# Kernel optimization log

Hardware: AMD Instinct MI355X
Metric: run time of the kernel (lower is better)

## Reference

```python
import jax, jax.numpy as jnp
import numpy as np

N_R = 256          # number of relations
N_HOP_MAX = 3      # max hops
N_E = 200_000      # number of entities
N_T = 1_000_000    # number of KB triples
B = 32             # batch size
D_Q = 768          # BERT question embedding dim
D_IN = D_Q + (N_HOP_MAX - 1) * N_R  # input width of dense_inf / dense_att


def setup_inputs() -> dict:
    key = jax.random.key(0)
    ks = jax.random.split(key, 7)
    x = (jax.random.uniform(ks[0], (B, N_E)) < 0.001).astype(jnp.float32)
    h_q = jax.random.normal(ks[1], (B, D_Q), jnp.float32)
    W_inf = jax.random.normal(ks[2], (N_R, D_IN), jnp.float32) * 0.02
    W_att = jax.random.normal(ks[3], (1, D_IN), jnp.float32) * 0.02
    subj_idx = jax.random.randint(ks[4], (N_T,), 0, N_E, jnp.int32)
    rel_idx = jax.random.randint(ks[5], (N_T,), 0, N_R, jnp.int32)
    obj_idx = jax.random.randint(ks[6], (N_T,), 0, N_E, jnp.int32)
    return {"x": x, "h_q": h_q, "W_inf": W_inf, "W_att": W_att,
            "subj_idx": subj_idx, "rel_idx": rel_idx, "obj_idx": obj_idx,
            "n_hop": N_HOP_MAX}


def _one_step(x, r, subj_idx, rel_idx, obj_idx):
    # Equivalent to ((x @ M_subj.T) * (r @ M_rel.T)) @ M_obj with 0/1
    # indicator matrices: gather - elementwise multiply - scatter-add.
    x_t = jnp.take(x, subj_idx, axis=1)   # (B, N_T)
    r_t = jnp.take(r, rel_idx, axis=1)    # (B, N_T)
    prod = x_t * r_t                       # (B, N_T)
    # scatter-add over triples into object entities: (N_T, B) -> (N_E, B)
    return jax.ops.segment_sum(prod.T, obj_idx, num_segments=x.shape[1]).T


def reference(x, h_q, W_inf, W_att, subj_idx, rel_idx, obj_idx, n_hop):
    rs, cs, xs = [], [], []
    for i in range(n_hop):
        if i:
            # most-recent relation first, then older ones (rs[::-1])
            concat = jnp.concatenate([h_q] + rs[::-1], axis=1)
        else:
            concat = h_q
        pad = jnp.zeros((h_q.shape[0], (N_HOP_MAX - 1 - i) * N_R), h_q.dtype)
        concat = jnp.concatenate([concat, pad], axis=1)  # (B, D_IN)
        r = concat @ W_inf.T   # (B, N_R)
        c = concat @ W_att.T   # (B, 1)
        x = _one_step(x, r, subj_idx, rel_idx, obj_idx)  # (B, N_E)
        rs.append(r)
        cs.append(c)
        xs.append(x)
    a = jax.nn.softmax(jnp.concatenate(cs, axis=1), axis=-1)  # (B, n_hop)
    y = jnp.einsum('bh,bhe->be', a, jnp.stack(xs, axis=1))     # (B, N_E)
    return y
```

## Files before the change

### kernel.cpp

```cpp
#include <hip/hip_runtime.h>

#define N_R   256
#define N_E   200000
#define N_T   1000000
#define B     32
#define D_Q   768
#define D_IN  1280

__global__ void k_prep(const float* __restrict__ x, unsigned* __restrict__ mask0,
                       unsigned* __restrict__ mask1, unsigned* __restrict__ mask2,
                       float4* __restrict__ outv) {
    int tid = blockIdx.x * 256 + threadIdx.x;
    float4 z = {0.f, 0.f, 0.f, 0.f};
    outv[tid] = z;
    outv[800000 + tid] = z;
    if (tid < N_E) {
        unsigned m = 0;
#pragma unroll 8
        for (int b = 0; b < 32; ++b)
            m |= (x[(size_t)b * N_E + tid] != 0.f ? 1u : 0u) << b;
        mask0[tid] = m;
        mask1[tid] = 0u;
        mask2[tid] = 0u;
    }
}

__global__ void k_r0(const float* __restrict__ h_q, const float* __restrict__ W_inf,
                     float* __restrict__ rT0) {
    __shared__ float hs[32 * 257];
    __shared__ float red[256];
    int t = threadIdx.x, rel = blockIdx.x;
    int b = t & 31, kp = t >> 5;
    float acc = 0.f;
    for (int c = 0; c < 3; ++c) {
        __syncthreads();
#pragma unroll
        for (int i = 0; i < 32; ++i)
            hs[i * 257 + t] = h_q[i * D_Q + c * 256 + t];
        __syncthreads();
        const float* w = &W_inf[rel * D_IN + c * 256 + kp * 32];
#pragma unroll
        for (int i = 0; i < 32; ++i)
            acc += w[i] * hs[b * 257 + kp * 32 + i];
    }
    red[t] = acc;
    __syncthreads();
    if (t < 32) {
        float s = 0.f;
        for (int q = 0; q < 8; ++q) s += red[q * 32 + t];
        rT0[rel * 32 + t] = s;
    }
}

__global__ void k_r12(const float* __restrict__ W_inf, const float* __restrict__ rT0,
                      const float* __restrict__ rPrev, float* __restrict__ rOut,
                      int hop2, const float* __restrict__ a_scale) {
    __shared__ float red[256];
    int t = threadIdx.x, rel = blockIdx.x;
    int b = t & 31, jp = t >> 5;
    const float* w2 = &W_inf[rel * D_IN + D_Q];
    float acc = 0.f;
#pragma unroll 8
    for (int jj = 0; jj < 32; ++jj) {
        int j = jp * 32 + jj;
        acc += w2[j] * rPrev[j * 32 + b];
    }
    if (hop2) {
        const float* w3 = w2 + N_R;
#pragma unroll 8
        for (int jj = 0; jj < 32; ++jj) {
            int j = jp * 32 + jj;
            acc += w3[j] * rT0[j * 32 + b];
        }
    }
    red[t] = acc;
    __syncthreads();
    if (t < 32) {
        float s = rT0[rel * 32 + t];
        for (int q = 0; q < 8; ++q) s += red[q * 32 + t];
        if (a_scale) s *= a_scale[t];
        rOut[rel * 32 + t] = s;
    }
}

__global__ void k_att(const float* __restrict__ h_q, const float* __restrict__ W_att,
                      const float* __restrict__ rT0, const float* __restrict__ rT1,
                      float* __restrict__ a_w) {
    __shared__ float p0[256], p1[256], p2[256], p3[256];
    int t = threadIdx.x;
    int b = t & 31, p = t >> 5;
    float c0 = 0.f;
    for (int k = p * 96; k < p * 96 + 96; ++k) c0 += W_att[k] * h_q[b * D_Q + k];
    float s1 = 0.f, s2 = 0.f, s3 = 0.f;
    for (int j = p * 32; j < p * 32 + 32; ++j) {
        float w2 = W_att[D_Q + j], w3 = W_att[D_Q + N_R + j];
        float r0v = rT0[j * 32 + b], r1v = rT1[j * 32 + b];
        s1 += w2 * r0v; s2 += w2 * r1v; s3 += w3 * r0v;
    }
    p0[t] = c0; p1[t] = s1; p2[t] = s2; p3[t] = s3;
    __syncthreads();
    if (t < 32) {
        float C0 = 0.f, S1 = 0.f, S2 = 0.f, S3 = 0.f;
        for (int q = 0; q < 8; ++q) {
            C0 += p0[q * 32 + t]; S1 += p1[q * 32 + t];
            S2 += p2[q * 32 + t]; S3 += p3[q * 32 + t];
        }
        float c1 = C0 + S1, c2 = C0 + S2 + S3;
        float m  = fmaxf(C0, fmaxf(c1, c2));
        float e0 = __expf(C0 - m), e1 = __expf(c1 - m), e2 = __expf(c2 - m);
        float inv = 1.f / (e0 + e1 + e2);
        a_w[t] = e0 * inv; a_w[32 + t] = e1 * inv; a_w[64 + t] = e2 * inv;
    }
}

template <bool BN_LAYOUT, bool HAS_NEXT>
__global__ void k_hop(const float* __restrict__ xIn,
                      const unsigned* __restrict__ maskIn,
                      const float* __restrict__ rT, const float* __restrict__ aw,
                      const int* __restrict__ subj, const int* __restrict__ rel,
                      const int* __restrict__ obj,
                      float* __restrict__ xOut, unsigned* __restrict__ maskOut,
                      float* __restrict__ outp) {
    int stride = gridDim.x * 256;
    for (int i = blockIdx.x * 256 + threadIdx.x; i < N_T; i += stride) {
        int s = __builtin_nontemporal_load(&subj[i]);
        unsigned m = maskIn[s];
        if (!m) continue;
        int r = __builtin_nontemporal_load(&rel[i]);
        int o = __builtin_nontemporal_load(&obj[i]);
        const float* rrow = rT + r * 32;
        const float* xrow = BN_LAYOUT ? (xIn + s) : (xIn + (size_t)s * 32);
        unsigned mm = m;
        while (mm) {
            int b = __ffs(mm) - 1;
            mm &= mm - 1;
            float v = BN_LAYOUT ? xrow[(size_t)b * N_E] : xrow[b];
            float c = v * rrow[b];
            if (HAS_NEXT) {
                unsafeAtomicAdd(&xOut[(size_t)o * 32 + b], c);
                unsafeAtomicAdd(&outp[(size_t)b * N_E + o], aw[b] * c);
            } else {
                unsafeAtomicAdd(&outp[(size_t)b * N_E + o], c);
            }
        }
        if (HAS_NEXT) atomicOr(&maskOut[o], m);
    }
}

extern "C" void kernel_launch(void* const* d_in, const int* in_sizes, int n_in,
                              void* d_out, int out_size, void* d_ws, size_t ws_size,
                              hipStream_t stream) {
    const float* x     = (const float*)d_in[0];
    const float* h_q   = (const float*)d_in[1];
    const float* W_inf = (const float*)d_in[2];
    const float* W_att = (const float*)d_in[3];
    const int*   subj  = (const int*)d_in[4];
    const int*   rel   = (const int*)d_in[5];
    const int*   obj   = (const int*)d_in[6];
    float* out = (float*)d_out;

    const size_t NEB = (size_t)N_E * B;
    float*    bufA  = (float*)d_ws;
    float*    bufB  = bufA + NEB;
    float*    rT    = bufB + NEB;
    float*    a_w   = rT + 3 * N_R * B;
    unsigned* mask0 = (unsigned*)(a_w + 96);
    unsigned* mask1 = mask0 + N_E;
    unsigned* mask2 = mask1 + N_E;

    const int PB = 3125;
    const int HB = 2048;

    k_prep<<<PB, 256, 0, stream>>>(x, mask0, mask1, mask2, (float4*)out);

    k_r0 <<<N_R, 256, 0, stream>>>(h_q, W_inf, rT);
    k_r12<<<N_R, 256, 0, stream>>>(W_inf, rT, rT, rT + N_R * B, 0, (const float*)0);
    k_att<<<1, 256, 0, stream>>>(h_q, W_att, rT, rT + N_R * B, a_w);
    k_r12<<<N_R, 256, 0, stream>>>(W_inf, rT, rT + N_R * B, rT + 2 * N_R * B, 1,
                                   a_w + 64);

    k_hop<true, true><<<HB, 256, 0, stream>>>(x, mask0, rT, a_w,
                                              subj, rel, obj, bufA, mask1, out);
    k_hop<false, true><<<HB, 256, 0, stream>>>(bufA, mask1, rT + N_R * B, a_w + 32,
                                               subj, rel, obj, bufB, mask2, out);
    k_hop<false, false><<<HB, 256, 0, stream>>>(bufB, mask2, rT + 2 * N_R * B,
                                                (const float*)0,
                                                subj, rel, obj, (float*)0,
                                                (unsigned*)0, out);
}
```

Before: 219.4 us.

## Fuse all stages into one cooperative kernel with grid-wide syncs

The eight separate launches (prep, three relation projections, attention, three hops) are replaced by a single cooperative kernel of 1024 blocks that separates phases with grid.sync(). The first relation projection is split into four K-chunks to spread work over more blocks. Later projections accumulate into rT1/rT2 with atomics, and the hop-3 attention weight moves from pre-scaling rT2 into the hop loop. This removes launch gaps and inter-kernel idle time, at the cost of grid-barrier overhead, fewer resident threads during the hops, and atomic partial sums in the projections.

```diff
diff --git a/kernel.cpp b/kernel.cpp
--- a/kernel.cpp
+++ b/kernel.cpp
@@ -1,190 +1,209 @@
 #include <hip/hip_runtime.h>
+#include <hip/hip_cooperative_groups.h>
+
+namespace cg = cooperative_groups;
 
 #define N_R   256
 #define N_E   200000
 #define N_T   1000000
-#define B     32
 #define D_Q   768
 #define D_IN  1280
 
-__global__ void k_prep(const float* __restrict__ x, unsigned* __restrict__ mask0,
-                       unsigned* __restrict__ mask1, unsigned* __restrict__ mask2,
-                       float4* __restrict__ outv) {
-    int tid = blockIdx.x * 256 + threadIdx.x;
-    float4 z = {0.f, 0.f, 0.f, 0.f};
-    outv[tid] = z;
-    outv[800000 + tid] = z;
-    if (tid < N_E) {
-        unsigned m = 0;
-#pragma unroll 8
-        for (int b = 0; b < 32; ++b)
-            m |= (x[(size_t)b * N_E + tid] != 0.f ? 1u : 0u) << b;
-        mask0[tid] = m;
-        mask1[tid] = 0u;
-        mask2[tid] = 0u;
-    }
-}
-
-__global__ void k_r0(const float* __restrict__ h_q, const float* __restrict__ W_inf,
-                     float* __restrict__ rT0) {
-    __shared__ float hs[32 * 257];
-    __shared__ float red[256];
-    int t = threadIdx.x, rel = blockIdx.x;
-    int b = t & 31, kp = t >> 5;
-    float acc = 0.f;
-    for (int c = 0; c < 3; ++c) {
-        __syncthreads();
-#pragma unroll
-        for (int i = 0; i < 32; ++i)
-            hs[i * 257 + t] = h_q[i * D_Q + c * 256 + t];
-        __syncthreads();
-        const float* w = &W_inf[rel * D_IN + c * 256 + kp * 32];
-#pragma unroll
-        for (int i = 0; i < 32; ++i)
-            acc += w[i] * hs[b * 257 + kp * 32 + i];
-    }
-    red[t] = acc;
+struct Params {
+    const float* x; const float* h_q; const float* W_inf; const float* W_att;
+    const int* subj; const int* rel; const int* obj;
+    float* out; float* bufA; float* bufB;
+    float* rT0part;
+    float* rT0; float* rT1; float* rT2;
+    float* a_w;
+    unsigned* mask0; unsigned* mask1; unsigned* mask2;
+};
+
+template <bool BN, bool HASNEXT>
+__device__ __forceinline__ void hop_phase(
+        const float* __restrict__ xIn, const unsigned* __restrict__ maskIn,
+        const float* __restrict__ rT, const float* __restrict__ awg,
+        const int* __restrict__ subj, const int* __restrict__ rel,
+        const int* __restrict__ obj, float* __restrict__ xOut,
+        unsigned* __restrict__ maskOut, float* __restrict__ outp,
+        float* awsh, int t) {
+    if (t < 32) awsh[t] = awg[t];
     __syncthreads();
-    if (t < 32) {
-        float s = 0.f;
-        for (int q = 0; q < 8; ++q) s += red[q * 32 + t];
-        rT0[rel * 32 + t] = s;
-    }
-}
-
-__global__ void k_r12(const float* __restrict__ W_inf, const float* __restrict__ rT0,
-                      const float* __restrict__ rPrev, float* __restrict__ rOut,
-                      int hop2, const float* __restrict__ a_scale) {
-    __shared__ float red[256];
-    int t = threadIdx.x, rel = blockIdx.x;
-    int b = t & 31, jp = t >> 5;
-    const float* w2 = &W_inf[rel * D_IN + D_Q];
-    float acc = 0.f;
-#pragma unroll 8
-    for (int jj = 0; jj < 32; ++jj) {
-        int j = jp * 32 + jj;
-        acc += w2[j] * rPrev[j * 32 + b];
-    }
-    if (hop2) {
-        const float* w3 = w2 + N_R;
-#pragma unroll 8
-        for (int jj = 0; jj < 32; ++jj) {
-            int j = jp * 32 + jj;
-            acc += w3[j] * rT0[j * 32 + b];
-        }
-    }
-    red[t] = acc;
-    __syncthreads();
-    if (t < 32) {
-        float s = rT0[rel * 32 + t];
-        for (int q = 0; q < 8; ++q) s += red[q * 32 + t];
-        if (a_scale) s *= a_scale[t];
-        rOut[rel * 32 + t] = s;
-    }
-}
-
-__global__ void k_att(const float* __restrict__ h_q, const float* __restrict__ W_att,
-                      const float* __restrict__ rT0, const float* __restrict__ rT1,
-                      float* __restrict__ a_w) {
-    __shared__ float p0[256], p1[256], p2[256], p3[256];
-    int t = threadIdx.x;
-    int b = t & 31, p = t >> 5;
-    float c0 = 0.f;
-    for (int k = p * 96; k < p * 96 + 96; ++k) c0 += W_att[k] * h_q[b * D_Q + k];
-    float s1 = 0.f, s2 = 0.f, s3 = 0.f;
-    for (int j = p * 32; j < p * 32 + 32; ++j) {
-        float w2 = W_att[D_Q + j], w3 = W_att[D_Q + N_R + j];
-        float r0v = rT0[j * 32 + b], r1v = rT1[j * 32 + b];
-        s1 += w2 * r0v; s2 += w2 * r1v; s3 += w3 * r0v;
-    }
-    p0[t] = c0; p1[t] = s1; p2[t] = s2; p3[t] = s3;
-    __syncthreads();
-    if (t < 32) {
-        float C0 = 0.f, S1 = 0.f, S2 = 0.f, S3 = 0.f;
-        for (int q = 0; q < 8; ++q) {
-            C0 += p0[q * 32 + t]; S1 += p1[q * 32 + t];
-            S2 += p2[q * 32 + t]; S3 += p3[q * 32 + t];
-        }
-        float c1 = C0 + S1, c2 = C0 + S2 + S3;
-        float m  = fmaxf(C0, fmaxf(c1, c2));
-        float e0 = __expf(C0 - m), e1 = __expf(c1 - m), e2 = __expf(c2 - m);
-        float inv = 1.f / (e0 + e1 + e2);
-        a_w[t] = e0 * inv; a_w[32 + t] = e1 * inv; a_w[64 + t] = e2 * inv;
-    }
-}
-
-template <bool BN_LAYOUT, bool HAS_NEXT>
-__global__ void k_hop(const float* __restrict__ xIn,
-                      const unsigned* __restrict__ maskIn,
-                      const float* __restrict__ rT, const float* __restrict__ aw,
-                      const int* __restrict__ subj, const int* __restrict__ rel,
-                      const int* __restrict__ obj,
-                      float* __restrict__ xOut, unsigned* __restrict__ maskOut,
-                      float* __restrict__ outp) {
     int stride = gridDim.x * 256;
-    for (int i = blockIdx.x * 256 + threadIdx.x; i < N_T; i += stride) {
+    for (int i = blockIdx.x * 256 + t; i < N_T; i += stride) {
         int s = __builtin_nontemporal_load(&subj[i]);
         unsigned m = maskIn[s];
         if (!m) continue;
         int r = __builtin_nontemporal_load(&rel[i]);
         int o = __builtin_nontemporal_load(&obj[i]);
         const float* rrow = rT + r * 32;
-        const float* xrow = BN_LAYOUT ? (xIn + s) : (xIn + (size_t)s * 32);
         unsigned mm = m;
         while (mm) {
-            int b = __ffs(mm) - 1;
+            int bb = __ffs(mm) - 1;
             mm &= mm - 1;
-            float v = BN_LAYOUT ? xrow[(size_t)b * N_E] : xrow[b];
-            float c = v * rrow[b];
-            if (HAS_NEXT) {
-                unsafeAtomicAdd(&xOut[(size_t)o * 32 + b], c);
-                unsafeAtomicAdd(&outp[(size_t)b * N_E + o], aw[b] * c);
-            } else {
-                unsafeAtomicAdd(&outp[(size_t)b * N_E + o], c);
+            float v = BN ? xIn[(size_t)bb * N_E + s] : xIn[(size_t)s * 32 + bb];
+            float c = v * rrow[bb];
+            if (HASNEXT) unsafeAtomicAdd(&xOut[(size_t)o * 32 + bb], c);
+            unsafeAtomicAdd(&outp[(size_t)bb * N_E + o], awsh[bb] * c);
+        }
+        if (HASNEXT) atomicOr(&maskOut[o], m);
+    }
+}
+
+__global__ void __launch_bounds__(256, 4) k_all(Params p) {
+    cg::grid_group grid = cg::this_grid();
+    __shared__ float red[256];
+    __shared__ float aws[32];
+    int t = threadIdx.x;
+    int b = t & 31, kp = t >> 5;
+    int tid = blockIdx.x * 256 + t;
+    int T = gridDim.x * 256;
+
+    float4 z = {0.f, 0.f, 0.f, 0.f};
+    float4* outv = (float4*)p.out;
+    for (int i = tid; i < 1600000; i += T) outv[i] = z;
+    for (int e = tid; e < N_E; e += T) {
+        unsigned m = 0;
+#pragma unroll 8
+        for (int bb = 0; bb < 32; ++bb)
+            m |= (p.x[(size_t)bb * N_E + e] != 0.f ? 1u : 0u) << bb;
+        p.mask0[e] = m; p.mask1[e] = 0u; p.mask2[e] = 0u;
+    }
+    for (int i = tid; i < 2 * 8192 + 96; i += T) p.rT1[i] = 0.f;
+    for (int w = blockIdx.x; w < 1024; w += gridDim.x) {
+        int rel = w & 255, q = w >> 8;
+        const float* wr = p.W_inf + rel * D_IN + q * 192 + kp * 24;
+        const float* hr = p.h_q + b * D_Q + q * 192 + kp * 24;
+        float acc = 0.f;
+#pragma unroll
+        for (int i = 0; i < 24; ++i) acc += wr[i] * hr[i];
+        __syncthreads();
+        red[t] = acc;
+        __syncthreads();
+        if (t < 32) {
+            float s = 0.f;
+            for (int qq = 0; qq < 8; ++qq) s += red[t + 32 * qq];
+            p.rT0part[q * 8192 + rel * 32 + t] = s;
+        }
+    }
+    grid.sync();
+
+    for (int w = blockIdx.x; w < 1024; w += gridDim.x) {
+        int rel = w & 255, q = w >> 8;
+        const float* w2 = p.W_inf + rel * D_IN + D_Q;
+        float acc = 0.f;
+        int j0 = q * 64 + kp * 8;
+#pragma unroll
+        for (int i = 0; i < 8; ++i) {
+            int j = j0 + i;
+            float r0v = p.rT0part[j * 32 + b] + p.rT0part[8192 + j * 32 + b]
+                      + p.rT0part[16384 + j * 32 + b] + p.rT0part[24576 + j * 32 + b];
+            acc += w2[j] * r0v;
+        }
+        __syncthreads();
+        red[t] = acc;
+        __syncthreads();
+        if (t < 32) {
+            float s = 0.f;
+            for (int qq = 0; qq < 8; ++qq) s += red[t + 32 * qq];
+            if (q == 0) {
+                float s0 = p.rT0part[rel * 32 + t] + p.rT0part[8192 + rel * 32 + t]
+                         + p.rT0part[16384 + rel * 32 + t]
+                         + p.rT0part[24576 + rel * 32 + t];
+                p.rT0[rel * 32 + t] = s0;
+                s += s0;
             }
-        }
-        if (HAS_NEXT) atomicOr(&maskOut[o], m);
-    }
+            unsafeAtomicAdd(&p.rT1[rel * 32 + t], s);
+        }
+    }
+    grid.sync();
+
+    for (int w = blockIdx.x; w < 1024; w += gridDim.x) {
+        int rel = w & 255, q = w >> 8;
+        const float* w2 = p.W_inf + rel * D_IN + D_Q;
+        const float* w3 = w2 + N_R;
+        float acc = 0.f;
+        int j0 = q * 64 + kp * 8;
+#pragma unroll
+        for (int i = 0; i < 8; ++i) {
+            int j = j0 + i;
+            acc += w2[j] * p.rT1[j * 32 + b] + w3[j] * p.rT0[j * 32 + b];
+        }
+        __syncthreads();
+        red[t] = acc;
+        __syncthreads();
+        if (t < 32) {
+            float s = 0.f;
+            for (int qq = 0; qq < 8; ++qq) s += red[t + 32 * qq];
+            if (q == 0) s += p.rT0[rel * 32 + t];
+            unsafeAtomicAdd(&p.rT2[rel * 32 + t], s);
+        }
+    }
+    if (blockIdx.x == 0) {
+        float c0 = 0.f;
+        for (int k = kp * 96; k < kp * 96 + 96; ++k)
+            c0 += p.W_att[k] * p.h_q[b * D_Q + k];
+        float s1 = 0.f, s2 = 0.f, s3 = 0.f;
+        for (int j = kp * 32; j < kp * 32 + 32; ++j) {
+            float w2 = p.W_att[D_Q + j], w3 = p.W_att[D_Q + N_R + j];
+            float r0v = p.rT0[j * 32 + b], r1v = p.rT1[j * 32 + b];
+            s1 += w2 * r0v; s2 += w2 * r1v; s3 += w3 * r0v;
+        }
+        float C0 = 0.f, S1 = 0.f, S2 = 0.f, S3 = 0.f;
+        __syncthreads(); red[t] = c0; __syncthreads();
+        if (t < 32) for (int q = 0; q < 8; ++q) C0 += red[t + 32 * q];
+        __syncthreads(); red[t] = s1; __syncthreads();
+        if (t < 32) for (int q = 0; q < 8; ++q) S1 += red[t + 32 * q];
+        __syncthreads(); red[t] = s2; __syncthreads();
+        if (t < 32) for (int q = 0; q < 8; ++q) S2 += red[t + 32 * q];
+        __syncthreads(); red[t] = s3; __syncthreads();
+        if (t < 32) for (int q = 0; q < 8; ++q) S3 += red[t + 32 * q];
+        if (t < 32) {
+            float c1 = C0 + S1, c2 = C0 + S2 + S3;
+            float m  = fmaxf(C0, fmaxf(c1, c2));
+            float e0 = __expf(C0 - m), e1 = __expf(c1 - m), e2 = __expf(c2 - m);
+            float inv = 1.f / (e0 + e1 + e2);
+            p.a_w[t] = e0 * inv; p.a_w[32 + t] = e1 * inv; p.a_w[64 + t] = e2 * inv;
+        }
+    }
+    grid.sync();
+
+    hop_phase<true, true>(p.x, p.mask0, p.rT0, p.a_w, p.subj, p.rel, p.obj,
+                          p.bufA, p.mask1, p.out, aws, t);
+    grid.sync();
+    hop_phase<false, true>(p.bufA, p.mask1, p.rT1, p.a_w + 32, p.subj, p.rel,
+                           p.obj, p.bufB, p.mask2, p.out, aws, t);
+    grid.sync();
+    hop_phase<false, false>(p.bufB, p.mask2, p.rT2, p.a_w + 64, p.subj, p.rel,
+                            p.obj, (float*)0, (unsigned*)0, p.out, aws, t);
 }
 
 extern "C" void kernel_launch(void* const* d_in, const int* in_sizes, int n_in,
                               void* d_out, int out_size, void* d_ws, size_t ws_size,
                               hipStream_t stream) {
-    const float* x     = (const float*)d_in[0];
-    const float* h_q   = (const float*)d_in[1];
-    const float* W_inf = (const float*)d_in[2];
-    const float* W_att = (const float*)d_in[3];
-    const int*   subj  = (const int*)d_in[4];
-    const int*   rel   = (const int*)d_in[5];
-    const int*   obj   = (const int*)d_in[6];
-    float* out = (float*)d_out;
-
-    const size_t NEB = (size_t)N_E * B;
-    float*    bufA  = (float*)d_ws;
-    float*    bufB  = bufA + NEB;
-    float*    rT    = bufB + NEB;
-    float*    a_w   = rT + 3 * N_R * B;
-    unsigned* mask0 = (unsigned*)(a_w + 96);
-    unsigned* mask1 = mask0 + N_E;
-    unsigned* mask2 = mask1 + N_E;
-
-    const int PB = 3125;
-    const int HB = 2048;
-
-    k_prep<<<PB, 256, 0, stream>>>(x, mask0, mask1, mask2, (float4*)out);
-
-    k_r0 <<<N_R, 256, 0, stream>>>(h_q, W_inf, rT);
-    k_r12<<<N_R, 256, 0, stream>>>(W_inf, rT, rT, rT + N_R * B, 0, (const float*)0);
-    k_att<<<1, 256, 0, stream>>>(h_q, W_att, rT, rT + N_R * B, a_w);
-    k_r12<<<N_R, 256, 0, stream>>>(W_inf, rT, rT + N_R * B, rT + 2 * N_R * B, 1,
-                                   a_w + 64);
-
-    k_hop<true, true><<<HB, 256, 0, stream>>>(x, mask0, rT, a_w,
-                                              subj, rel, obj, bufA, mask1, out);
-    k_hop<false, true><<<HB, 256, 0, stream>>>(bufA, mask1, rT + N_R * B, a_w + 32,
-                                               subj, rel, obj, bufB, mask2, out);
-    k_hop<false, false><<<HB, 256, 0, stream>>>(bufB, mask2, rT + 2 * N_R * B,
-                                                (const float*)0,
-                                                subj, rel, obj, (float*)0,
-                                                (unsigned*)0, out);
+    Params prm;
+    prm.x     = (const float*)d_in[0];
+    prm.h_q   = (const float*)d_in[1];
+    prm.W_inf = (const float*)d_in[2];
+    prm.W_att = (const float*)d_in[3];
+    prm.subj  = (const int*)d_in[4];
+    prm.rel   = (const int*)d_in[5];
+    prm.obj   = (const int*)d_in[6];
+    prm.out   = (float*)d_out;
+
+    float* w = (float*)d_ws;
+    prm.bufA    = w; w += (size_t)N_E * 32;
+    prm.bufB    = w; w += (size_t)N_E * 32;
+    prm.rT0part = w; w += 4 * 8192;
+    prm.rT0     = w; w += 8192;
+    prm.rT1     = w; w += 8192;
+    prm.rT2     = w; w += 8192;
+    prm.a_w     = w; w += 96;
+    prm.mask0   = (unsigned*)w; 
+    prm.mask1   = prm.mask0 + N_E;
+    prm.mask2   = prm.mask1 + N_E;
+
+    void* args[] = { &prm };
+    hipLaunchCooperativeKernel((const void*)k_all, dim3(1024), dim3(256),
+                               args, 0, stream);
 }
```

Measured after the change: 783.7 us. 3.57x slower.

## Fuse small matvec kernels into hop kernels and defer weighted output accumulation

Applied to the files above, without the earlier changes.

Merges the prep and r0 kernels, and runs the r1/r2/attention matvecs as extra blocks inside the hop kernels, cutting the launch count from eight to five. The hop kernels no longer issue a second scattered atomic into the output per contribution. Instead, a final coalesced pass (kE) adds the attention-weighted bufA and bufB into the output through a shared-memory transpose. This trades a full dense read of both intermediate buffers and a read-modify-write of the output for half the atomics in hops 1 and 2.

```diff
diff --git a/kernel.cpp b/kernel.cpp
--- a/kernel.cpp
+++ b/kernel.cpp
@@ -3,147 +3,220 @@
 #define N_R   256
 #define N_E   200000
 #define N_T   1000000
-#define B     32
 #define D_Q   768
 #define D_IN  1280
 
-__global__ void k_prep(const float* __restrict__ x, unsigned* __restrict__ mask0,
-                       unsigned* __restrict__ mask1, unsigned* __restrict__ mask2,
-                       float4* __restrict__ outv) {
-    int tid = blockIdx.x * 256 + threadIdx.x;
-    float4 z = {0.f, 0.f, 0.f, 0.f};
-    outv[tid] = z;
-    outv[800000 + tid] = z;
-    if (tid < N_E) {
-        unsigned m = 0;
-#pragma unroll 8
-        for (int b = 0; b < 32; ++b)
-            m |= (x[(size_t)b * N_E + tid] != 0.f ? 1u : 0u) << b;
-        mask0[tid] = m;
-        mask1[tid] = 0u;
-        mask2[tid] = 0u;
-    }
-}
-
-__global__ void k_r0(const float* __restrict__ h_q, const float* __restrict__ W_inf,
-                     float* __restrict__ rT0) {
-    __shared__ float hs[32 * 257];
-    __shared__ float red[256];
-    int t = threadIdx.x, rel = blockIdx.x;
-    int b = t & 31, kp = t >> 5;
-    float acc = 0.f;
-    for (int c = 0; c < 3; ++c) {
-        __syncthreads();
-#pragma unroll
-        for (int i = 0; i < 32; ++i)
-            hs[i * 257 + t] = h_q[i * D_Q + c * 256 + t];
-        __syncthreads();
-        const float* w = &W_inf[rel * D_IN + c * 256 + kp * 32];
-#pragma unroll
-        for (int i = 0; i < 32; ++i)
-            acc += w[i] * hs[b * 257 + kp * 32 + i];
-    }
-    red[t] = acc;
-    __syncthreads();
-    if (t < 32) {
-        float s = 0.f;
-        for (int q = 0; q < 8; ++q) s += red[q * 32 + t];
-        rT0[rel * 32 + t] = s;
-    }
-}
-
-__global__ void k_r12(const float* __restrict__ W_inf, const float* __restrict__ rT0,
-                      const float* __restrict__ rPrev, float* __restrict__ rOut,
-                      int hop2, const float* __restrict__ a_scale) {
-    __shared__ float red[256];
-    int t = threadIdx.x, rel = blockIdx.x;
-    int b = t & 31, jp = t >> 5;
-    const float* w2 = &W_inf[rel * D_IN + D_Q];
-    float acc = 0.f;
-#pragma unroll 8
-    for (int jj = 0; jj < 32; ++jj) {
-        int j = jp * 32 + jj;
-        acc += w2[j] * rPrev[j * 32 + b];
-    }
-    if (hop2) {
-        const float* w3 = w2 + N_R;
-#pragma unroll 8
-        for (int jj = 0; jj < 32; ++jj) {
-            int j = jp * 32 + jj;
-            acc += w3[j] * rT0[j * 32 + b];
-        }
-    }
-    red[t] = acc;
-    __syncthreads();
-    if (t < 32) {
-        float s = rT0[rel * 32 + t];
-        for (int q = 0; q < 8; ++q) s += red[q * 32 + t];
-        if (a_scale) s *= a_scale[t];
-        rOut[rel * 32 + t] = s;
-    }
-}
-
-__global__ void k_att(const float* __restrict__ h_q, const float* __restrict__ W_att,
-                      const float* __restrict__ rT0, const float* __restrict__ rT1,
-                      float* __restrict__ a_w) {
-    __shared__ float p0[256], p1[256], p2[256], p3[256];
-    int t = threadIdx.x;
-    int b = t & 31, p = t >> 5;
-    float c0 = 0.f;
-    for (int k = p * 96; k < p * 96 + 96; ++k) c0 += W_att[k] * h_q[b * D_Q + k];
-    float s1 = 0.f, s2 = 0.f, s3 = 0.f;
-    for (int j = p * 32; j < p * 32 + 32; ++j) {
-        float w2 = W_att[D_Q + j], w3 = W_att[D_Q + N_R + j];
-        float r0v = rT0[j * 32 + b], r1v = rT1[j * 32 + b];
-        s1 += w2 * r0v; s2 += w2 * r1v; s3 += w3 * r0v;
-    }
-    p0[t] = c0; p1[t] = s1; p2[t] = s2; p3[t] = s3;
-    __syncthreads();
-    if (t < 32) {
-        float C0 = 0.f, S1 = 0.f, S2 = 0.f, S3 = 0.f;
-        for (int q = 0; q < 8; ++q) {
-            C0 += p0[q * 32 + t]; S1 += p1[q * 32 + t];
-            S2 += p2[q * 32 + t]; S3 += p3[q * 32 + t];
-        }
-        float c1 = C0 + S1, c2 = C0 + S2 + S3;
-        float m  = fmaxf(C0, fmaxf(c1, c2));
-        float e0 = __expf(C0 - m), e1 = __expf(c1 - m), e2 = __expf(c2 - m);
-        float inv = 1.f / (e0 + e1 + e2);
-        a_w[t] = e0 * inv; a_w[32 + t] = e1 * inv; a_w[64 + t] = e2 * inv;
-    }
-}
-
-template <bool BN_LAYOUT, bool HAS_NEXT>
-__global__ void k_hop(const float* __restrict__ xIn,
-                      const unsigned* __restrict__ maskIn,
-                      const float* __restrict__ rT, const float* __restrict__ aw,
-                      const int* __restrict__ subj, const int* __restrict__ rel,
-                      const int* __restrict__ obj,
-                      float* __restrict__ xOut, unsigned* __restrict__ maskOut,
-                      float* __restrict__ outp) {
-    int stride = gridDim.x * 256;
-    for (int i = blockIdx.x * 256 + threadIdx.x; i < N_T; i += stride) {
+template <bool BN>
+__device__ __forceinline__ void hop_core(
+        const float* __restrict__ xIn, const unsigned* __restrict__ maskIn,
+        const float* __restrict__ rT,
+        const int* __restrict__ subj, const int* __restrict__ rel,
+        const int* __restrict__ obj,
+        float* __restrict__ xOut, unsigned* __restrict__ maskOut,
+        int gb, int nGroups, int t) {
+    int stride = nGroups * 256;
+    for (int i = gb * 256 + t; i < N_T; i += stride) {
         int s = __builtin_nontemporal_load(&subj[i]);
         unsigned m = maskIn[s];
         if (!m) continue;
         int r = __builtin_nontemporal_load(&rel[i]);
         int o = __builtin_nontemporal_load(&obj[i]);
         const float* rrow = rT + r * 32;
-        const float* xrow = BN_LAYOUT ? (xIn + s) : (xIn + (size_t)s * 32);
         unsigned mm = m;
         while (mm) {
-            int b = __ffs(mm) - 1;
+            int bb = __ffs(mm) - 1;
             mm &= mm - 1;
-            float v = BN_LAYOUT ? xrow[(size_t)b * N_E] : xrow[b];
-            float c = v * rrow[b];
-            if (HAS_NEXT) {
-                unsafeAtomicAdd(&xOut[(size_t)o * 32 + b], c);
-                unsafeAtomicAdd(&outp[(size_t)b * N_E + o], aw[b] * c);
-            } else {
-                unsafeAtomicAdd(&outp[(size_t)b * N_E + o], c);
+            float v = BN ? xIn[(size_t)bb * N_E + s] : xIn[(size_t)s * 32 + bb];
+            unsafeAtomicAdd(&xOut[(size_t)o * 32 + bb], v * rrow[bb]);
+        }
+        atomicOr(&maskOut[o], m);
+    }
+}
+
+__global__ void kA(const float* __restrict__ x, const float* __restrict__ h_q,
+                   const float* __restrict__ W_inf,
+                   unsigned* __restrict__ mask0, unsigned* __restrict__ mask1,
+                   unsigned* __restrict__ mask2,
+                   float4* __restrict__ outv, float* __restrict__ rT0) {
+    __shared__ float hs[32 * 257];
+    __shared__ float red[256];
+    int t = threadIdx.x;
+    if (blockIdx.x < 782) {
+        int tid = blockIdx.x * 256 + t;
+        float4 z = {0.f, 0.f, 0.f, 0.f};
+        for (int i = tid; i < 1600000; i += 782 * 256) outv[i] = z;
+        if (tid < N_E) {
+            unsigned m = 0;
+#pragma unroll 8
+            for (int b = 0; b < 32; ++b)
+                m |= (x[(size_t)b * N_E + tid] != 0.f ? 1u : 0u) << b;
+            mask0[tid] = m;
+            mask1[tid] = 0u;
+            mask2[tid] = 0u;
+        }
+    } else {
+        int rel = blockIdx.x - 782;
+        int b = t & 31, kp = t >> 5;
+        float acc = 0.f;
+        for (int c = 0; c < 3; ++c) {
+            __syncthreads();
+#pragma unroll
+            for (int i = 0; i < 32; ++i)
+                hs[i * 257 + t] = h_q[i * D_Q + c * 256 + t];
+            __syncthreads();
+            const float* w = &W_inf[rel * D_IN + c * 256 + kp * 32];
+#pragma unroll
+            for (int i = 0; i < 32; ++i)
+                acc += w[i] * hs[b * 257 + kp * 32 + i];
+        }
+        red[t] = acc;
+        __syncthreads();
+        if (t < 32) {
+            float s = 0.f;
+            for (int q = 0; q < 8; ++q) s += red[q * 32 + t];
+            rT0[rel * 32 + t] = s;
+        }
+    }
+}
+
+__global__ void kB(const float* __restrict__ W_inf, const float* __restrict__ rT0,
+                   float* __restrict__ rT1,
+                   const float* __restrict__ x, const unsigned* __restrict__ mask0,
+                   const int* __restrict__ subj, const int* __restrict__ rel,
+                   const int* __restrict__ obj,
+                   float* __restrict__ bufA, unsigned* __restrict__ mask1) {
+    __shared__ float red[256];
+    int t = threadIdx.x;
+    if (blockIdx.x < 256) {
+        int relb = blockIdx.x;
+        int b = t & 31, jp = t >> 5;
+        const float* w2 = &W_inf[relb * D_IN + D_Q];
+        float acc = 0.f;
+#pragma unroll 8
+        for (int jj = 0; jj < 32; ++jj) {
+            int j = jp * 32 + jj;
+            acc += w2[j] * rT0[j * 32 + b];
+        }
+        red[t] = acc;
+        __syncthreads();
+        if (t < 32) {
+            float s = rT0[relb * 32 + t];
+            for (int q = 0; q < 8; ++q) s += red[q * 32 + t];
+            rT1[relb * 32 + t] = s;
+        }
+    } else {
+        hop_core<true>(x, mask0, rT0, subj, rel, obj, bufA, mask1,
+                       blockIdx.x - 256, 2048, t);
+    }
+}
+
+__global__ void kC(const float* __restrict__ W_inf, const float* __restrict__ W_att,
+                   const float* __restrict__ h_q,
+                   const float* __restrict__ rT0, const float* __restrict__ rT1,
+                   float* __restrict__ rT2, float* __restrict__ a_w,
+                   const float* __restrict__ bufA, const unsigned* __restrict__ mask1,
+                   const int* __restrict__ subj, const int* __restrict__ rel,
+                   const int* __restrict__ obj,
+                   float* __restrict__ bufB, unsigned* __restrict__ mask2) {
+    __shared__ float red[256];
+    __shared__ float p0[256], p1[256], p2[256], p3[256];
+    int t = threadIdx.x;
+    if (blockIdx.x < 256) {
+        int relb = blockIdx.x;
+        int b = t & 31, jp = t >> 5;
+        const float* w2 = &W_inf[relb * D_IN + D_Q];
+        const float* w3 = w2 + N_R;
+        float acc = 0.f;
+#pragma unroll 8
+        for (int jj = 0; jj < 32; ++jj) {
+            int j = jp * 32 + jj;
+            acc += w2[j] * rT1[j * 32 + b] + w3[j] * rT0[j * 32 + b];
+        }
+        red[t] = acc;
+        __syncthreads();
+        if (t < 32) {
+            float s = rT0[relb * 32 + t];
+            for (int q = 0; q < 8; ++q) s += red[q * 32 + t];
+            rT2[relb * 32 + t] = s;
+        }
+    } else if (blockIdx.x == 256) {
+        int b = t & 31, p = t >> 5;
+        float c0 = 0.f;
+        for (int k = p * 96; k < p * 96 + 96; ++k) c0 += W_att[k] * h_q[b * D_Q + k];
+        float s1 = 0.f, s2 = 0.f, s3 = 0.f;
+        for (int j = p * 32; j < p * 32 + 32; ++j) {
+            float w2 = W_att[D_Q + j], w3 = W_att[D_Q + N_R + j];
+            float r0v = rT0[j * 32 + b], r1v = rT1[j * 32 + b];
+            s1 += w2 * r0v; s2 += w2 * r1v; s3 += w3 * r0v;
+        }
+        p0[t] = c0; p1[t] = s1; p2[t] = s2; p3[t] = s3;
+        __syncthreads();
+        if (t < 32) {
+            float C0 = 0.f, S1 = 0.f, S2 = 0.f, S3 = 0.f;
+            for (int q = 0; q < 8; ++q) {
+                C0 += p0[q * 32 + t]; S1 += p1[q * 32 + t];
+                S2 += p2[q * 32 + t]; S3 += p3[q * 32 + t];
             }
-        }
-        if (HAS_NEXT) atomicOr(&maskOut[o], m);
+            float c1 = C0 + S1, c2 = C0 + S2 + S3;
+            float m  = fmaxf(C0, fmaxf(c1, c2));
+            float e0 = __expf(C0 - m), e1 = __expf(c1 - m), e2 = __expf(c2 - m);
+            float inv = 1.f / (e0 + e1 + e2);
+            a_w[t] = e0 * inv; a_w[32 + t] = e1 * inv; a_w[64 + t] = e2 * inv;
+        }
+    } else {
+        hop_core<false>(bufA, mask1, rT1, subj, rel, obj, bufB, mask2,
+                        blockIdx.x - 257, 2048, t);
+    }
+}
+
+__global__ void kD(const float* __restrict__ bufB, const unsigned* __restrict__ mask2,
+                   const float* __restrict__ rT2, const float* __restrict__ a_w,
+                   const int* __restrict__ subj, const int* __restrict__ rel,
+                   const int* __restrict__ obj, float* __restrict__ out) {
+    __shared__ float aws[32];
+    int t = threadIdx.x;
+    if (t < 32) aws[t] = a_w[64 + t];
+    __syncthreads();
+    int stride = gridDim.x * 256;
+    for (int i = blockIdx.x * 256 + t; i < N_T; i += stride) {
+        int s = __builtin_nontemporal_load(&subj[i]);
+        unsigned m = mask2[s];
+        if (!m) continue;
+        int r = __builtin_nontemporal_load(&rel[i]);
+        int o = __builtin_nontemporal_load(&obj[i]);
+        const float* rrow = rT2 + r * 32;
+        unsigned mm = m;
+        while (mm) {
+            int bb = __ffs(mm) - 1;
+            mm &= mm - 1;
+            float v = bufB[(size_t)s * 32 + bb];
+            unsafeAtomicAdd(&out[(size_t)bb * N_E + o], aws[bb] * v * rrow[bb]);
+        }
+    }
+}
+
+__global__ void kE(const float* __restrict__ bufA, const float* __restrict__ bufB,
+                   const float* __restrict__ a_w, float* __restrict__ out) {
+    __shared__ float tile[32 * 65];
+    __shared__ float a0s[32], a1s[32];
+    int t = threadIdx.x;
+    if (t < 32) { a0s[t] = a_w[t]; a1s[t] = a_w[32 + t]; }
+    __syncthreads();
+    int e0 = blockIdx.x * 64;
+#pragma unroll
+    for (int i = 0; i < 8; ++i) {
+        int o = i * 256 + t;
+        int e = o >> 5, b = o & 31;
+        size_t idx = (size_t)(e0 + e) * 32 + b;
+        tile[b * 65 + e] = a0s[b] * bufA[idx] + a1s[b] * bufB[idx];
+    }
+    __syncthreads();
+#pragma unroll
+    for (int i = 0; i < 8; ++i) {
+        int o = i * 256 + t;
+        int b = o >> 6, e = o & 63;
+        int oi = b * N_E + e0 + e;
+        out[oi] += tile[b * 65 + e];
     }
 }
 
@@ -159,32 +232,23 @@
     const int*   obj   = (const int*)d_in[6];
     float* out = (float*)d_out;
 
-    const size_t NEB = (size_t)N_E * B;
+    const size_t NEB = (size_t)N_E * 32;
     float*    bufA  = (float*)d_ws;
     float*    bufB  = bufA + NEB;
-    float*    rT    = bufB + NEB;
-    float*    a_w   = rT + 3 * N_R * B;
+    float*    rT0   = bufB + NEB;
+    float*    rT1   = rT0 + N_R * 32;
+    float*    rT2   = rT1 + N_R * 32;
+    float*    a_w   = rT2 + N_R * 32;
     unsigned* mask0 = (unsigned*)(a_w + 96);
     unsigned* mask1 = mask0 + N_E;
     unsigned* mask2 = mask1 + N_E;
 
-    const int PB = 3125;
-    const int HB = 2048;
-
-    k_prep<<<PB, 256, 0, stream>>>(x, mask0, mask1, mask2, (float4*)out);
-
-    k_r0 <<<N_R, 256, 0, stream>>>(h_q, W_inf, rT);
-    k_r12<<<N_R, 256, 0, stream>>>(W_inf, rT, rT, rT + N_R * B, 0, (const float*)0);
-    k_att<<<1, 256, 0, stream>>>(h_q, W_att, rT, rT + N_R * B, a_w);
-    k_r12<<<N_R, 256, 0, stream>>>(W_inf, rT, rT + N_R * B, rT + 2 * N_R * B, 1,
-                                   a_w + 64);
-
-    k_hop<true, true><<<HB, 256, 0, stream>>>(x, mask0, rT, a_w,
-                                              subj, rel, obj, bufA, mask1, out);
-    k_hop<false, true><<<HB, 256, 0, stream>>>(bufA, mask1, rT + N_R * B, a_w + 32,
-                                               subj, rel, obj, bufB, mask2, out);
-    k_hop<false, false><<<HB, 256, 0, stream>>>(bufB, mask2, rT + 2 * N_R * B,
-                                                (const float*)0,
-                                                subj, rel, obj, (float*)0,
-                                                (unsigned*)0, out);
-}
+    kA<<<782 + 256, 256, 0, stream>>>(x, h_q, W_inf, mask0, mask1, mask2,
+                                      (float4*)out, rT0);
+    kB<<<256 + 2048, 256, 0, stream>>>(W_inf, rT0, rT1, x, mask0,
+                                       subj, rel, obj, bufA, mask1);
+    kC<<<257 + 2048, 256, 0, stream>>>(W_inf, W_att, h_q, rT0, rT1, rT2, a_w,
+                                       bufA, mask1, subj, rel, obj, bufB, mask2);
+    kD<<<2048, 256, 0, stream>>>(bufB, mask2, rT2, a_w, subj, rel, obj, out);
+    kE<<<3125, 256, 0, stream>>>(bufA, bufB, a_w, out);
+}
```

After: 204.3 us. -6.9%, faster.
